# Performance work log

Measured on AMD Instinct MI355X. Metric: run time of the kernel, lower is better.

## Reference

```python
import jax, jax.numpy as jnp
import numpy as np

B, T, C = 4, 2048, 384
NUM_HEADS, HEAD_SIZE = 6, 64


def setup_inputs() -> dict:
    key = jax.random.key(0)
    ks = jax.random.split(key, 6)
    s = 1.0 / np.sqrt(C)
    return {
        "x": jax.random.normal(ks[0], (B, T, C), dtype=jnp.float32),
        "Wq": jax.random.normal(ks[1], (C, NUM_HEADS * HEAD_SIZE), dtype=jnp.float32) * s,
        "bq": jnp.zeros((NUM_HEADS * HEAD_SIZE,), dtype=jnp.float32),
        "Wk": jax.random.normal(ks[2], (C, NUM_HEADS * HEAD_SIZE), dtype=jnp.float32) * s,
        "bk": jnp.zeros((NUM_HEADS * HEAD_SIZE,), dtype=jnp.float32),
        "Wv": jax.random.normal(ks[3], (C, NUM_HEADS * HEAD_SIZE), dtype=jnp.float32) * s,
        "bv": jnp.zeros((NUM_HEADS * HEAD_SIZE,), dtype=jnp.float32),
        "Wo": jax.random.normal(ks[4], (NUM_HEADS * HEAD_SIZE, C), dtype=jnp.float32) * s,
        "bo": jnp.zeros((C,), dtype=jnp.float32),
    }


def reference(x, Wq, bq, Wk, bk, Wv, bv, Wo, bo):
    b, t, c = x.shape
    h, d = NUM_HEADS, HEAD_SIZE
    q = (x @ Wq + bq).reshape(b, t, h, d)
    k = (x @ Wk + bk).reshape(b, t, h, d)
    v = (x @ Wv + bv).reshape(b, t, h, d)
    scores = jnp.einsum('bthd,bshd->bhts', q, k) / jnp.sqrt(jnp.float32(d))
    causal = jnp.tril(jnp.ones((t, t), dtype=bool))  # [t,t]
    scores = jnp.where(causal, scores, -jnp.inf)
    weights = jax.nn.softmax(scores, axis=-1)  # dropout identity (inference)
    ctx = jnp.einsum('bhts,bshd->bthd', weights, v).reshape(b, t, h * d)
    return ctx @ Wo + bo
```

## Files before the change

kernel.cpp:

```cpp
#include <hip/hip_runtime.h>

#define B_  4
#define T_  2048
#define C_  384
#define NH_ 6
#define HS_ 64
#define M_  (B_*T_)

typedef float floatx4 __attribute__((ext_vector_type(4)));
typedef __bf16 bf16x8 __attribute__((ext_vector_type(8)));
typedef unsigned short ushort_t;
typedef unsigned short ushortx8 __attribute__((ext_vector_type(8)));
typedef unsigned short ushortx4 __attribute__((ext_vector_type(4)));
typedef unsigned int uintx2 __attribute__((ext_vector_type(2)));

__device__ __forceinline__ ushort_t f2bf(float f) {
    unsigned u = __builtin_bit_cast(unsigned, f);
    unsigned r = (u + 0x7FFFu + ((u >> 16) & 1u)) >> 16;
    return (ushort_t)r;
}
__device__ __forceinline__ unsigned f2bf_pk(float lo, float hi) {
    return (__builtin_bit_cast(unsigned, lo) >> 16) |
           (__builtin_bit_cast(unsigned, hi) & 0xFFFF0000u);
}

__global__ __launch_bounds__(256) void prep(
    const float* __restrict__ x, ushort_t* __restrict__ xb,
    const float* __restrict__ Wq, const float* __restrict__ Wk,
    const float* __restrict__ Wv, const float* __restrict__ Wo,
    ushort_t* __restrict__ Wtq, ushort_t* __restrict__ Wtk,
    ushort_t* __restrict__ Wtv, ushort_t* __restrict__ Wto)
{
    __shared__ float Ls[64][65];
    const int tid = threadIdx.x;
    const int bx = blockIdx.x;

    if (bx < 1536) {
        const int i = (bx * 256 + tid) * 8;
        const float4 a = *(const float4*)&x[i];
        const float4 b = *(const float4*)&x[i + 4];
        ushortx8 p;
        p[0] = f2bf(a.x); p[1] = f2bf(a.y); p[2] = f2bf(a.z); p[3] = f2bf(a.w);
        p[4] = f2bf(b.x); p[5] = f2bf(b.y); p[6] = f2bf(b.z); p[7] = f2bf(b.w);
        *(ushortx8*)&xb[i] = p;
        return;
    }

    const int idx = bx - 1536;
    const int z = idx / 36, rest = idx % 36;
    const float* __restrict__ W = (z == 0) ? Wq : (z == 1) ? Wk : (z == 2) ? Wv : Wo;
    ushort_t* __restrict__ Wt   = (z == 0) ? Wtq : (z == 1) ? Wtk : (z == 2) ? Wtv : Wto;
    const int k0 = (rest / 6) * 64, n0 = (rest % 6) * 64;

    #pragma unroll
    for (int p = 0; p < 4; ++p) {
        const int kk = p * 16 + (tid >> 4);
        const int nn = (tid & 15) * 4;
        const float4 v = *(const float4*)&W[(size_t)(k0 + kk) * 384 + n0 + nn];
        Ls[kk][nn] = v.x; Ls[kk][nn + 1] = v.y; Ls[kk][nn + 2] = v.z; Ls[kk][nn + 3] = v.w;
    }
    __syncthreads();
    #pragma unroll
    for (int p = 0; p < 4; ++p) {
        const int n = p * 16 + (tid >> 4);
        const int kc = (tid & 15) * 4;
        ushortx4 pk;
        #pragma unroll
        for (int t = 0; t < 4; ++t) pk[t] = f2bf(Ls[kc + t][n]);
        *(ushortx4*)&Wt[(size_t)(n0 + n) * 384 + k0 + kc] = pk;
    }
}

__global__ __launch_bounds__(256) void qkv_gemm(
    const ushort_t* __restrict__ xb,
    const ushort_t* __restrict__ Wtq, const ushort_t* __restrict__ Wtk,
    const ushort_t* __restrict__ Wtv,
    const float* __restrict__ bq, const float* __restrict__ bk, const float* __restrict__ bv,
    ushort_t* __restrict__ Qb, ushort_t* __restrict__ Kb, ushort_t* __restrict__ Vtb)
{
    __shared__ ushort_t Sm[2][6144];

    const int tid  = threadIdx.x;
    const int lane = tid & 63;
    const int wv   = tid >> 6;
    const int m    = lane & 15;
    const int quad = lane >> 4;

    const int t0 = blockIdx.x * 64;
    const int n0 = blockIdx.y * 128;
    const int which = n0 / 384;
    const int n_in0 = n0 % 384;
    const bool isV = (which == 2);

    const ushort_t* __restrict__ Wt = (which == 0) ? Wtq : (which == 1) ? Wtk : Wtv;

    const int tg0 = (wv & 1) * 32;
    const int ng0 = (wv >> 1) * 64;

    const int rX = tid >> 2, cX = tid & 3;
    const int swX = ((cX ^ ((rX >> 1) & 3)) << 3);
    const int rW0 = tid >> 2, rW1 = rW0 + 64, cW = tid & 3;
    const int swW = ((cW ^ ((rW0 >> 1) & 3)) << 3);

    floatx4 acc[8];
    #pragma unroll
    for (int i = 0; i < 8; ++i) acc[i] = (floatx4){0.f, 0.f, 0.f, 0.f};

    ushortx8 xr  = *(const ushortx8*)&xb[(size_t)(t0 + rX) * 384 + cX * 8];
    ushortx8 wr0 = *(const ushortx8*)&Wt[(size_t)(n_in0 + rW0) * 384 + cW * 8];
    ushortx8 wr1 = *(const ushortx8*)&Wt[(size_t)(n_in0 + rW1) * 384 + cW * 8];

    for (int ks = 0; ks < 12; ++ks) {
        ushort_t* __restrict__ S = &Sm[ks & 1][0];
        *(ushortx8*)&S[rX * 32 + swX] = xr;
        *(ushortx8*)&S[2048 + rW0 * 32 + swW] = wr0;
        *(ushortx8*)&S[2048 + rW1 * 32 + swW] = wr1;
        __syncthreads();

        if (ks < 11) {
            const int kk = (ks + 1) * 32;
            xr  = *(const ushortx8*)&xb[(size_t)(t0 + rX) * 384 + kk + cX * 8];
            wr0 = *(const ushortx8*)&Wt[(size_t)(n_in0 + rW0) * 384 + kk + cW * 8];
            wr1 = *(const ushortx8*)&Wt[(size_t)(n_in0 + rW1) * 384 + kk + cW * 8];
        }

        bf16x8 fX[2], fW[4];
        #pragma unroll
        for (int i = 0; i < 2; ++i) {
            const int r = tg0 + i * 16 + m;
            fX[i] = *(const bf16x8*)&S[r * 32 + ((quad ^ ((r >> 1) & 3)) << 3)];
        }
        #pragma unroll
        for (int i = 0; i < 4; ++i) {
            const int r = ng0 + i * 16 + m;
            fW[i] = *(const bf16x8*)&S[2048 + r * 32 + ((quad ^ ((r >> 1) & 3)) << 3)];
        }
        if (isV) {
            #pragma unroll
            for (int i = 0; i < 2; ++i)
                #pragma unroll
                for (int j = 0; j < 4; ++j)
                    acc[i * 4 + j] = __builtin_amdgcn_mfma_f32_16x16x32_bf16(fX[i], fW[j], acc[i * 4 + j], 0, 0, 0);
        } else {
            #pragma unroll
            for (int i = 0; i < 4; ++i)
                #pragma unroll
                for (int j = 0; j < 2; ++j)
                    acc[i * 2 + j] = __builtin_amdgcn_mfma_f32_16x16x32_bf16(fW[i], fX[j], acc[i * 2 + j], 0, 0, 0);
        }
    }

    if (!isV) {
        ushort_t* __restrict__ out = (which == 0) ? Qb : Kb;
        const float* __restrict__ bias = (which == 0) ? bq : bk;
        const float scale = (which == 0) ? 0.125f : 1.0f;
        #pragma unroll
        for (int i = 0; i < 4; ++i) {
            const int n_base = n_in0 + ng0 + i * 16 + quad * 4;
            const int h = n_base >> 6, d0 = n_base & 63;
            #pragma unroll
            for (int j = 0; j < 2; ++j) {
                const int tg = t0 + tg0 + j * 16 + m;
                const int b = tg >> 11, tb = tg & (T_ - 1);
                ushortx4 pk;
                #pragma unroll
                for (int r = 0; r < 4; ++r)
                    pk[r] = f2bf((acc[i * 2 + j][r] + bias[n_base + r]) * scale);
                *(ushortx4*)&out[(((size_t)(b * NH_ + h)) * T_ + tb) * HS_ + d0] = pk;
            }
        }
    } else {
        #pragma unroll
        for (int i = 0; i < 2; ++i) {
            const int tgq = t0 + tg0 + i * 16 + quad * 4;
            const int b = tgq >> 11, tb0 = tgq & (T_ - 1);
            #pragma unroll
            for (int j = 0; j < 4; ++j) {
                const int n_l = n_in0 + ng0 + j * 16 + m;
                const int h = n_l >> 6, d = n_l & 63;
                const float bb = bv[n_l];
                ushortx4 pk;
                #pragma unroll
                for (int r = 0; r < 4; ++r) pk[r] = f2bf(acc[i * 4 + j][r] + bb);
                *(ushortx4*)&Vtb[(((size_t)(b * NH_ + h)) * HS_ + d) * T_ + tb0] = pk;
            }
        }
    }
}

__global__ __launch_bounds__(256) void proj_gemm(
    const ushort_t* __restrict__ ctxb,
    const ushort_t* __restrict__ Wto,
    const float* __restrict__ bo,
    float* __restrict__ out)
{
    __shared__ ushort_t Sm[2][4096];

    const int tid  = threadIdx.x;
    const int lane = tid & 63;
    const int wv   = tid >> 6;
    const int m    = lane & 15;
    const int quad = lane >> 4;

    const int t0 = blockIdx.x * 64;
    const int n0 = blockIdx.y * 64;
    const int tg0 = (wv & 1) * 32;
    const int ng0 = (wv >> 1) * 32;

    const int rC = tid >> 2, cC = tid & 3;
    const int swC = ((cC ^ ((rC >> 1) & 3)) << 3);

    floatx4 acc[2][2];
    #pragma unroll
    for (int i = 0; i < 2; ++i)
        #pragma unroll
        for (int j = 0; j < 2; ++j) acc[i][j] = (floatx4){0.f, 0.f, 0.f, 0.f};

    ushortx8 cr = *(const ushortx8*)&ctxb[(size_t)(t0 + rC) * 384 + cC * 8];
    ushortx8 wr = *(const ushortx8*)&Wto[(size_t)(n0 + rC) * 384 + cC * 8];

    for (int ks = 0; ks < 12; ++ks) {
        ushort_t* __restrict__ S = &Sm[ks & 1][0];
        *(ushortx8*)&S[rC * 32 + swC] = cr;
        *(ushortx8*)&S[2048 + rC * 32 + swC] = wr;
        __syncthreads();

        if (ks < 11) {
            const int kk = (ks + 1) * 32;
            cr = *(const ushortx8*)&ctxb[(size_t)(t0 + rC) * 384 + kk + cC * 8];
            wr = *(const ushortx8*)&Wto[(size_t)(n0 + rC) * 384 + kk + cC * 8];
        }

        bf16x8 fA[2], fB[2];
        #pragma unroll
        for (int i = 0; i < 2; ++i) {
            const int rn = ng0 + i * 16 + m;
            fA[i] = *(const bf16x8*)&S[2048 + rn * 32 + ((quad ^ ((rn >> 1) & 3)) << 3)];
            const int rt = tg0 + i * 16 + m;
            fB[i] = *(const bf16x8*)&S[rt * 32 + ((quad ^ ((rt >> 1) & 3)) << 3)];
        }
        #pragma unroll
        for (int i = 0; i < 2; ++i)
            #pragma unroll
            for (int j = 0; j < 2; ++j)
                acc[i][j] = __builtin_amdgcn_mfma_f32_16x16x32_bf16(fA[i], fB[j], acc[i][j], 0, 0, 0);
    }

    #pragma unroll
    for (int i = 0; i < 2; ++i) {
        const int n_base = n0 + ng0 + i * 16 + quad * 4;
        const float4 bb = *(const float4*)&bo[n_base];
        #pragma unroll
        for (int j = 0; j < 2; ++j) {
            const int tg = t0 + tg0 + j * 16 + m;
            float4 o;
            o.x = acc[i][j][0] + bb.x;
            o.y = acc[i][j][1] + bb.y;
            o.z = acc[i][j][2] + bb.z;
            o.w = acc[i][j][3] + bb.w;
            *(float4*)&out[(size_t)tg * 384 + n_base] = o;
        }
    }
}

__global__ __launch_bounds__(256) void attn_mfma(
    const ushort_t* __restrict__ Q,
    const ushort_t* __restrict__ K,
    const ushort_t* __restrict__ Vt,
    ushort_t* __restrict__ ctx)
{
    __shared__ ushort_t Ks[2][64 * 64];
    __shared__ ushort_t Vs[2][64 * 64];
    __shared__ ushort_t Ps[4][16 * 64];

    const int tid  = threadIdx.x;
    const int lane = tid & 63;
    const int wv   = tid >> 6;
    const int m    = lane & 15;
    const int quad = lane >> 4;
    const int cA   = (quad ^ (m & 7)) << 3;

    const int flat = blockIdx.x + 32 * (blockIdx.y + 6 * blockIdx.z);
    const int rr = flat >> 8, ss = flat & 255;
    const int rank = (rr << 8) + ((rr & 1) ? (255 - ss) : ss);
    const int j   = 31 - (rank / 24);
    const int idx = rank % 24;
    const int b   = idx / 6, h = idx % 6;
    const int bh  = idx;

    const int rowbase = j * 64 + wv * 16;
    const int ext = j;
    const int qloc = wv * 16 + m;

    const ushort_t* __restrict__ Kg = K  + (size_t)bh * (T_ * HS_);
    const ushort_t* __restrict__ Vg = Vt + (size_t)bh * (HS_ * T_);

    const int r0 = tid >> 3,         c0 = tid & 7;
    const int r1 = (tid + 256) >> 3, c1 = tid & 7;
    const int sw0 = ((c0 ^ (r0 & 7)) << 3);
    const int sw1 = ((c1 ^ (r1 & 7)) << 3);

    bf16x8 qf0, qf1;
    {
        const ushort_t* qp = Q + ((size_t)bh * T_ + rowbase + m) * HS_;
        qf0 = *(const bf16x8*)(qp + quad * 8);
        qf1 = *(const bf16x8*)(qp + 32 + quad * 8);
    }

    floatx4 acc_o[4];
    #pragma unroll
    for (int dt = 0; dt < 4; ++dt) acc_o[dt] = (floatx4){0.f, 0.f, 0.f, 0.f};
    float l_lane = 0.f;

    ushort_t* __restrict__ Pw = &Ps[wv][0];
    const int pbase = m * 64 + ((quad & 1) << 2);
    const int pcs   = (quad >> 1);
    const int pxor  = m & 7;

    ushortx8 kr0 = *(const ushortx8*)&Kg[(size_t)r0 * HS_ + c0 * 8];
    ushortx8 kr1 = *(const ushortx8*)&Kg[(size_t)r1 * HS_ + c1 * 8];
    ushortx8 vr0 = *(const ushortx8*)&Vg[(size_t)r0 * T_ + c0 * 8];
    ushortx8 vr1 = *(const ushortx8*)&Vg[(size_t)r1 * T_ + c1 * 8];

    for (int kt = 0; kt <= ext; ++kt) {
        ushort_t* __restrict__ Kc = &Ks[kt & 1][0];
        ushort_t* __restrict__ Vc = &Vs[kt & 1][0];
        *(ushortx8*)&Kc[r0 * 64 + sw0] = kr0;
        *(ushortx8*)&Kc[r1 * 64 + sw1] = kr1;
        *(ushortx8*)&Vc[r0 * 64 + sw0] = vr0;
        *(ushortx8*)&Vc[r1 * 64 + sw1] = vr1;
        __syncthreads();

        if (kt < ext) {
            const int s1 = (kt + 1) * 64;
            kr0 = *(const ushortx8*)&Kg[(size_t)(s1 + r0) * HS_ + c0 * 8];
            kr1 = *(const ushortx8*)&Kg[(size_t)(s1 + r1) * HS_ + c1 * 8];
            vr0 = *(const ushortx8*)&Vg[(size_t)r0 * T_ + s1 + c0 * 8];
            vr1 = *(const ushortx8*)&Vg[(size_t)r1 * T_ + s1 + c1 * 8];
        }

        floatx4 st[4];
        #pragma unroll
        for (int kc = 0; kc < 4; ++kc) {
            const int kb = (kc * 16 + m) * 64;
            bf16x8 k0 = *(const bf16x8*)&Kc[kb + cA];
            bf16x8 k1 = *(const bf16x8*)&Kc[kb + (cA ^ 32)];
            floatx4 a = (floatx4){0.f, 0.f, 0.f, 0.f};
            a = __builtin_amdgcn_mfma_f32_16x16x32_bf16(k0, qf0, a, 0, 0, 0);
            a = __builtin_amdgcn_mfma_f32_16x16x32_bf16(k1, qf1, a, 0, 0, 0);
            st[kc] = a;
        }

        if (kt == ext) {
            #pragma unroll
            for (int kc = 0; kc < 4; ++kc) {
                #pragma unroll
                for (int r = 0; r < 4; ++r)
                    if (kc * 16 + quad * 4 + r > qloc) st[kc][r] = -1e30f;
            }
        }

        float lsum = 0.f;
        #pragma unroll
        for (int kc = 0; kc < 4; ++kc) {
            const float p0 = __expf(st[kc][0]);
            const float p1 = __expf(st[kc][1]);
            const float p2 = __expf(st[kc][2]);
            const float p3 = __expf(st[kc][3]);
            lsum += (p0 + p1) + (p2 + p3);
            uintx2 pk;
            pk[0] = f2bf_pk(p0, p1);
            pk[1] = f2bf_pk(p2, p3);
            *(uintx2*)&Pw[pbase + (((kc * 2 + pcs) ^ pxor) << 3)] = pk;
        }
        l_lane += lsum;

        asm volatile("s_waitcnt lgkmcnt(0)" ::: "memory");
        bf16x8 pf0 = *(const bf16x8*)&Pw[m * 64 + cA];
        bf16x8 pf1 = *(const bf16x8*)&Pw[m * 64 + (cA ^ 32)];

        #pragma unroll
        for (int dt = 0; dt < 4; ++dt) {
            const int vb = (dt * 16 + m) * 64;
            bf16x8 v0 = *(const bf16x8*)&Vc[vb + cA];
            bf16x8 v1 = *(const bf16x8*)&Vc[vb + (cA ^ 32)];
            acc_o[dt] = __builtin_amdgcn_mfma_f32_16x16x32_bf16(v0, pf0, acc_o[dt], 0, 0, 0);
            acc_o[dt] = __builtin_amdgcn_mfma_f32_16x16x32_bf16(v1, pf1, acc_o[dt], 0, 0, 0);
        }
    }

    float ls = l_lane;
    ls += __shfl_xor(ls, 16, 64);
    ls += __shfl_xor(ls, 32, 64);
    const float rcp = 1.0f / ls;

    const int t = rowbase + m;
    ushort_t* __restrict__ cp = ctx + ((size_t)(b * T_) + t) * C_ + h * HS_ + quad * 4;
    #pragma unroll
    for (int dt = 0; dt < 4; ++dt) {
        ushortx4 pk;
        #pragma unroll
        for (int r = 0; r < 4; ++r) pk[r] = f2bf(acc_o[dt][r] * rcp);
        *(ushortx4*)&cp[dt * 16] = pk;
    }
}

extern "C" void kernel_launch(void* const* d_in, const int* in_sizes, int n_in,
                              void* d_out, int out_size, void* d_ws, size_t ws_size,
                              hipStream_t stream) {
    const float* x  = (const float*)d_in[0];
    const float* Wq = (const float*)d_in[1];
    const float* bq = (const float*)d_in[2];
    const float* Wk = (const float*)d_in[3];
    const float* bk = (const float*)d_in[4];
    const float* Wv = (const float*)d_in[5];
    const float* bv = (const float*)d_in[6];
    const float* Wo = (const float*)d_in[7];
    const float* bo = (const float*)d_in[8];
    float* out = (float*)d_out;

    const size_t per = (size_t)B_ * NH_ * T_ * HS_;
    const size_t wsz = 384 * 384;
    ushort_t* xb  = (ushort_t*)d_ws;
    ushort_t* Wtq = xb + per;
    ushort_t* Wtk = Wtq + wsz;
    ushort_t* Wtv = Wtk + wsz;
    ushort_t* Wto = Wtv + wsz;
    ushort_t* Qb  = Wto + wsz;
    ushort_t* Kb  = Qb + per;
    ushort_t* Vtb = Kb + per;
    ushort_t* ctxb = Vtb + per;

    prep<<<dim3(1536 + 144), 256, 0, stream>>>(
        x, xb, Wq, Wk, Wv, Wo, Wtq, Wtk, Wtv, Wto);

    qkv_gemm<<<dim3(M_ / 64, 1152 / 128), 256, 0, stream>>>(
        xb, Wtq, Wtk, Wtv, bq, bk, bv, Qb, Kb, Vtb);

    attn_mfma<<<dim3(32, NH_, B_), 256, 0, stream>>>(Qb, Kb, Vtb, ctxb);

    proj_gemm<<<dim3(M_ / 64, 384 / 64), 256, 0, stream>>>(ctxb, Wto, bo, out);
}
```

Measured before the change: 141.6 us.

## Process two query tiles per attention block to reuse K/V loads

Each attention block now handles 128 query rows (two 64-row tiles) instead of 64. Every K/V tile staged in shared memory feeds both tiles' MFMAs, which halves global K/V traffic and barrier count per query row. The grid shrinks from 768 to 384 blocks in a simple longest-first order, and the earlier serpentine block remapping is dropped. Costs are more registers (double accumulators and Q fragments), possibly lower occupancy, and a cruder load balance across causal lengths.

```diff
diff --git a/kernel.cpp b/kernel.cpp
--- a/kernel.cpp
+++ b/kernel.cpp
@@ -271,7 +271,7 @@
 {
     __shared__ ushort_t Ks[2][64 * 64];
     __shared__ ushort_t Vs[2][64 * 64];
-    __shared__ ushort_t Ps[4][16 * 64];
+    __shared__ ushort_t Ps[4][2][16 * 64];
 
     const int tid  = threadIdx.x;
     const int lane = tid & 63;
@@ -280,16 +280,12 @@
     const int quad = lane >> 4;
     const int cA   = (quad ^ (m & 7)) << 3;
 
-    const int flat = blockIdx.x + 32 * (blockIdx.y + 6 * blockIdx.z);
-    const int rr = flat >> 8, ss = flat & 255;
-    const int rank = (rr << 8) + ((rr & 1) ? (255 - ss) : ss);
-    const int j   = 31 - (rank / 24);
-    const int idx = rank % 24;
-    const int b   = idx / 6, h = idx % 6;
-    const int bh  = idx;
-
-    const int rowbase = j * 64 + wv * 16;
-    const int ext = j;
+    const int bx = blockIdx.x;
+    const int j  = 15 - (bx / 24);
+    const int bh = bx % 24;
+    const int b  = bh / 6, h = bh % 6;
+
+    const int ext  = 2 * j + 1;
     const int qloc = wv * 16 + m;
 
     const ushort_t* __restrict__ Kg = K  + (size_t)bh * (T_ * HS_);
@@ -300,19 +296,23 @@
     const int sw0 = ((c0 ^ (r0 & 7)) << 3);
     const int sw1 = ((c1 ^ (r1 & 7)) << 3);
 
-    bf16x8 qf0, qf1;
-    {
-        const ushort_t* qp = Q + ((size_t)bh * T_ + rowbase + m) * HS_;
-        qf0 = *(const bf16x8*)(qp + quad * 8);
-        qf1 = *(const bf16x8*)(qp + 32 + quad * 8);
-    }
-
-    floatx4 acc_o[4];
-    #pragma unroll
-    for (int dt = 0; dt < 4; ++dt) acc_o[dt] = (floatx4){0.f, 0.f, 0.f, 0.f};
-    float l_lane = 0.f;
-
-    ushort_t* __restrict__ Pw = &Ps[wv][0];
+    bf16x8 qf[2][2];
+    #pragma unroll
+    for (int rt = 0; rt < 2; ++rt) {
+        const ushort_t* qp = Q + ((size_t)bh * T_ + (j * 128 + rt * 64 + wv * 16 + m)) * HS_;
+        qf[rt][0] = *(const bf16x8*)(qp + quad * 8);
+        qf[rt][1] = *(const bf16x8*)(qp + 32 + quad * 8);
+    }
+
+    floatx4 acc_o[2][4];
+    #pragma unroll
+    for (int rt = 0; rt < 2; ++rt)
+        #pragma unroll
+        for (int dt = 0; dt < 4; ++dt) acc_o[rt][dt] = (floatx4){0.f, 0.f, 0.f, 0.f};
+    float l_lane[2] = {0.f, 0.f};
+
+    ushort_t* __restrict__ Pw0 = &Ps[wv][0][0];
+    ushort_t* __restrict__ Pw1 = &Ps[wv][1][0];
     const int pbase = m * 64 + ((quad & 1) << 2);
     const int pcs   = (quad >> 1);
     const int pxor  = m & 7;
@@ -339,69 +339,113 @@
             vr1 = *(const ushortx8*)&Vg[(size_t)r1 * T_ + s1 + c1 * 8];
         }
 
-        floatx4 st[4];
+        const bool do0 = (kt < ext);
+
+        floatx4 st0[4], st1[4];
         #pragma unroll
         for (int kc = 0; kc < 4; ++kc) {
             const int kb = (kc * 16 + m) * 64;
             bf16x8 k0 = *(const bf16x8*)&Kc[kb + cA];
             bf16x8 k1 = *(const bf16x8*)&Kc[kb + (cA ^ 32)];
-            floatx4 a = (floatx4){0.f, 0.f, 0.f, 0.f};
-            a = __builtin_amdgcn_mfma_f32_16x16x32_bf16(k0, qf0, a, 0, 0, 0);
-            a = __builtin_amdgcn_mfma_f32_16x16x32_bf16(k1, qf1, a, 0, 0, 0);
-            st[kc] = a;
-        }
-
+            if (do0) {
+                floatx4 a = (floatx4){0.f, 0.f, 0.f, 0.f};
+                a = __builtin_amdgcn_mfma_f32_16x16x32_bf16(k0, qf[0][0], a, 0, 0, 0);
+                a = __builtin_amdgcn_mfma_f32_16x16x32_bf16(k1, qf[0][1], a, 0, 0, 0);
+                st0[kc] = a;
+            }
+            floatx4 a1 = (floatx4){0.f, 0.f, 0.f, 0.f};
+            a1 = __builtin_amdgcn_mfma_f32_16x16x32_bf16(k0, qf[1][0], a1, 0, 0, 0);
+            a1 = __builtin_amdgcn_mfma_f32_16x16x32_bf16(k1, qf[1][1], a1, 0, 0, 0);
+            st1[kc] = a1;
+        }
+
+        if (kt == ext - 1) {
+            #pragma unroll
+            for (int kc = 0; kc < 4; ++kc)
+                #pragma unroll
+                for (int r = 0; r < 4; ++r)
+                    if (kc * 16 + quad * 4 + r > qloc) st0[kc][r] = -1e30f;
+        }
         if (kt == ext) {
             #pragma unroll
+            for (int kc = 0; kc < 4; ++kc)
+                #pragma unroll
+                for (int r = 0; r < 4; ++r)
+                    if (kc * 16 + quad * 4 + r > qloc) st1[kc][r] = -1e30f;
+        }
+
+        if (do0) {
+            float lsum = 0.f;
+            #pragma unroll
             for (int kc = 0; kc < 4; ++kc) {
-                #pragma unroll
-                for (int r = 0; r < 4; ++r)
-                    if (kc * 16 + quad * 4 + r > qloc) st[kc][r] = -1e30f;
-            }
-        }
-
-        float lsum = 0.f;
-        #pragma unroll
-        for (int kc = 0; kc < 4; ++kc) {
-            const float p0 = __expf(st[kc][0]);
-            const float p1 = __expf(st[kc][1]);
-            const float p2 = __expf(st[kc][2]);
-            const float p3 = __expf(st[kc][3]);
-            lsum += (p0 + p1) + (p2 + p3);
-            uintx2 pk;
-            pk[0] = f2bf_pk(p0, p1);
-            pk[1] = f2bf_pk(p2, p3);
-            *(uintx2*)&Pw[pbase + (((kc * 2 + pcs) ^ pxor) << 3)] = pk;
-        }
-        l_lane += lsum;
+                const float p0 = __expf(st0[kc][0]);
+                const float p1 = __expf(st0[kc][1]);
+                const float p2 = __expf(st0[kc][2]);
+                const float p3 = __expf(st0[kc][3]);
+                lsum += (p0 + p1) + (p2 + p3);
+                uintx2 pk;
+                pk[0] = f2bf_pk(p0, p1);
+                pk[1] = f2bf_pk(p2, p3);
+                *(uintx2*)&Pw0[pbase + (((kc * 2 + pcs) ^ pxor) << 3)] = pk;
+            }
+            l_lane[0] += lsum;
+        }
+        {
+            float lsum = 0.f;
+            #pragma unroll
+            for (int kc = 0; kc < 4; ++kc) {
+                const float p0 = __expf(st1[kc][0]);
+                const float p1 = __expf(st1[kc][1]);
+                const float p2 = __expf(st1[kc][2]);
+                const float p3 = __expf(st1[kc][3]);
+                lsum += (p0 + p1) + (p2 + p3);
+                uintx2 pk;
+                pk[0] = f2bf_pk(p0, p1);
+                pk[1] = f2bf_pk(p2, p3);
+                *(uintx2*)&Pw1[pbase + (((kc * 2 + pcs) ^ pxor) << 3)] = pk;
+            }
+            l_lane[1] += lsum;
+        }
 
         asm volatile("s_waitcnt lgkmcnt(0)" ::: "memory");
-        bf16x8 pf0 = *(const bf16x8*)&Pw[m * 64 + cA];
-        bf16x8 pf1 = *(const bf16x8*)&Pw[m * 64 + (cA ^ 32)];
+        bf16x8 pf00, pf01, pf10, pf11;
+        if (do0) {
+            pf00 = *(const bf16x8*)&Pw0[m * 64 + cA];
+            pf01 = *(const bf16x8*)&Pw0[m * 64 + (cA ^ 32)];
+        }
+        pf10 = *(const bf16x8*)&Pw1[m * 64 + cA];
+        pf11 = *(const bf16x8*)&Pw1[m * 64 + (cA ^ 32)];
 
         #pragma unroll
         for (int dt = 0; dt < 4; ++dt) {
             const int vb = (dt * 16 + m) * 64;
             bf16x8 v0 = *(const bf16x8*)&Vc[vb + cA];
             bf16x8 v1 = *(const bf16x8*)&Vc[vb + (cA ^ 32)];
-            acc_o[dt] = __builtin_amdgcn_mfma_f32_16x16x32_bf16(v0, pf0, acc_o[dt], 0, 0, 0);
-            acc_o[dt] = __builtin_amdgcn_mfma_f32_16x16x32_bf16(v1, pf1, acc_o[dt], 0, 0, 0);
-        }
-    }
-
-    float ls = l_lane;
-    ls += __shfl_xor(ls, 16, 64);
-    ls += __shfl_xor(ls, 32, 64);
-    const float rcp = 1.0f / ls;
-
-    const int t = rowbase + m;
-    ushort_t* __restrict__ cp = ctx + ((size_t)(b * T_) + t) * C_ + h * HS_ + quad * 4;
-    #pragma unroll
-    for (int dt = 0; dt < 4; ++dt) {
-        ushortx4 pk;
-        #pragma unroll
-        for (int r = 0; r < 4; ++r) pk[r] = f2bf(acc_o[dt][r] * rcp);
-        *(ushortx4*)&cp[dt * 16] = pk;
+            if (do0) {
+                acc_o[0][dt] = __builtin_amdgcn_mfma_f32_16x16x32_bf16(v0, pf00, acc_o[0][dt], 0, 0, 0);
+                acc_o[0][dt] = __builtin_amdgcn_mfma_f32_16x16x32_bf16(v1, pf01, acc_o[0][dt], 0, 0, 0);
+            }
+            acc_o[1][dt] = __builtin_amdgcn_mfma_f32_16x16x32_bf16(v0, pf10, acc_o[1][dt], 0, 0, 0);
+            acc_o[1][dt] = __builtin_amdgcn_mfma_f32_16x16x32_bf16(v1, pf11, acc_o[1][dt], 0, 0, 0);
+        }
+    }
+
+    #pragma unroll
+    for (int rt = 0; rt < 2; ++rt) {
+        float ls = l_lane[rt];
+        ls += __shfl_xor(ls, 16, 64);
+        ls += __shfl_xor(ls, 32, 64);
+        const float rcp = 1.0f / ls;
+
+        const int t = j * 128 + rt * 64 + wv * 16 + m;
+        ushort_t* __restrict__ cp = ctx + ((size_t)(b * T_) + t) * C_ + h * HS_ + quad * 4;
+        #pragma unroll
+        for (int dt = 0; dt < 4; ++dt) {
+            ushortx4 pk;
+            #pragma unroll
+            for (int r = 0; r < 4; ++r) pk[r] = f2bf(acc_o[rt][dt][r] * rcp);
+            *(ushortx4*)&cp[dt * 16] = pk;
+        }
     }
 }
 
@@ -437,7 +481,7 @@
     qkv_gemm<<<dim3(M_ / 64, 1152 / 128), 256, 0, stream>>>(
         xb, Wtq, Wtk, Wtv, bq, bk, bv, Qb, Kb, Vtb);
 
-    attn_mfma<<<dim3(32, NH_, B_), 256, 0, stream>>>(Qb, Kb, Vtb, ctxb);
+    attn_mfma<<<dim3(384), 256, 0, stream>>>(Qb, Kb, Vtb, ctxb);
 
     proj_gemm<<<dim3(M_ / 64, 384 / 64), 256, 0, stream>>>(ctxb, Wto, bo, out);
 }
```

After: 157.0 us. 10.8% more time.
